# Performance work log

Measured on AMD Instinct MI355X. Metric: run time of the kernel, lower is better.

Reference implementation:

```python
import jax, jax.numpy as jnp
import numpy as np

NUM_USER = 150000
NUM_ITEM = 75000
N = NUM_USER + NUM_ITEM
D = 64
NNZ = 2000000
GCN_LAYER = 3
SCALE = 0.01


def setup_inputs() -> dict:
    key = jax.random.key(0)
    ks = jax.random.split(key, 8)
    user_emb = jax.random.normal(ks[0], (NUM_USER, D), dtype=jnp.float32) * 0.01
    item_emb = jax.random.normal(ks[1], (NUM_ITEM, D), dtype=jnp.float32) * 0.01
    eps_weight = jax.random.normal(ks[2], (D, D), dtype=jnp.float32)
    eps_bias = jnp.zeros((D,), dtype=jnp.float32)
    adj_rows = jax.random.randint(ks[3], (NNZ,), 0, N, dtype=jnp.int32)
    adj_cols = jax.random.randint(ks[4], (NNZ,), 0, N, dtype=jnp.int32)
    # small positive values, mimicking symmetric-normalized adjacency entries
    adj_vals = jax.random.uniform(ks[5], (NNZ,), dtype=jnp.float32) * 0.1
    noise1 = jax.random.normal(ks[6], (N, D), dtype=jnp.float32)
    noise2 = jax.random.normal(ks[7], (N, D), dtype=jnp.float32)
    return {
        "user_emb": user_emb, "item_emb": item_emb,
        "eps_weight": eps_weight, "eps_bias": eps_bias,
        "adj_rows": adj_rows, "adj_cols": adj_cols, "adj_vals": adj_vals,
        "noise1": noise1, "noise2": noise2, "gcn_layer": GCN_LAYER,
    }


def _spmm(rows, cols, vals, x):
    # y[r] = sum_{e: rows[e]==r} vals[e] * x[cols[e]]  -- sparse adj @ x
    msgs = vals[:, None] * x[cols]          # [nnz, D]
    return jax.ops.segment_sum(msgs, rows, num_segments=N)


def reference(user_emb, item_emb, eps_weight, eps_bias,
              adj_rows, adj_cols, adj_vals, noise1, noise2, gcn_layer):
    ego = jnp.concatenate([user_emb, item_emb], axis=0)  # [N, D]
    acc = jnp.zeros_like(ego)
    for _ in range(gcn_layer):
        ego = _spmm(adj_rows, adj_cols, adj_vals, ego)
        acc = acc + ego
    mean = acc / gcn_layer                               # mean over stacked layers
    logstd = mean @ eps_weight + eps_bias
    std = jnp.exp(logstd)
    view1 = mean + std * noise1 * SCALE
    view2 = mean + std * noise2 * SCALE
    return (mean, std, view1, view2)
```

## Files before the change

### kernel.cpp

```cpp
#include <hip/hip_runtime.h>
#include <math.h>

#define NUM_USER 150000
#define NUM_ITEM 75000
#define N_TOTAL  225000
#define D        64
#define LAYERS   3
#define SCALE    0.01f

#define BROWS    128
#define BSHIFT   7
#define NBUCK    1758
#define COLBITS  18
#define COLMASK  0x3FFFF
#define CHUNK    8192

__global__ void k_zero(int* __restrict__ p, int n) {
    for (int i = blockIdx.x * blockDim.x + threadIdx.x; i < n;
         i += gridDim.x * blockDim.x)
        p[i] = 0;
}

__global__ __launch_bounds__(256) void k_binhist(const int* __restrict__ rows,
                                                 int* __restrict__ bcnt, int nnz) {
    __shared__ int h[NBUCK];
    const int tid = threadIdx.x;
    for (int i = tid; i < NBUCK; i += 256) h[i] = 0;
    __syncthreads();
    for (int e = blockIdx.x * blockDim.x + tid; e < nnz;
         e += gridDim.x * blockDim.x)
        atomicAdd(&h[rows[e] >> BSHIFT], 1);
    __syncthreads();
    for (int i = tid; i < NBUCK; i += 256)
        if (h[i]) atomicAdd(&bcnt[i], h[i]);
}

__global__ __launch_bounds__(256) void k_bscan(const int* __restrict__ bcnt,
                                               int* __restrict__ boff,
                                               int* __restrict__ bcur,
                                               int n, int nnz) {
    __shared__ int sd[256];
    const int t = threadIdx.x;
    const int base = t * 8;
    int v[8], s = 0;
#pragma unroll
    for (int i = 0; i < 8; ++i) {
        int idx = base + i;
        v[i] = (idx < n) ? bcnt[idx] : 0;
        s += v[i];
    }
    sd[t] = s;
    __syncthreads();
#pragma unroll
    for (int o = 1; o < 256; o <<= 1) {
        int x = (t >= o) ? sd[t - o] : 0;
        __syncthreads();
        if (t >= o) sd[t] += x;
        __syncthreads();
    }
    int run = (t == 0) ? 0 : sd[t - 1];
#pragma unroll
    for (int i = 0; i < 8; ++i) {
        int idx = base + i;
        if (idx < n) { boff[idx] = run; bcur[idx] = run; }
        run += v[i];
    }
    if (t == 255) boff[n] = nnz;
}

__global__ __launch_bounds__(256) void k_binscatter(
        const int* __restrict__ rows, const int* __restrict__ cols,
        const float* __restrict__ vals, int* __restrict__ bcur,
        uint2* __restrict__ rec, int nnz) {
    __shared__ int hist[NBUCK];
    __shared__ int runs[NBUCK];
    const int tid = threadIdx.x;
    const int e0 = blockIdx.x * CHUNK;
    const int e1 = min(nnz, e0 + CHUNK);

    for (int i = tid; i < NBUCK; i += 256) hist[i] = 0;
    __syncthreads();
    for (int e = e0 + tid; e < e1; e += 256)
        atomicAdd(&hist[rows[e] >> BSHIFT], 1);
    __syncthreads();
    for (int i = tid; i < NBUCK; i += 256)
        runs[i] = hist[i] ? atomicAdd(&bcur[i], hist[i]) : 0;
    __syncthreads();
    for (int i = tid; i < NBUCK; i += 256) hist[i] = 0;
    __syncthreads();
    for (int e = e0 + tid; e < e1; e += 256) {
        const int r = rows[e];
        const int b = r >> BSHIFT;
        const int pos = runs[b] + atomicAdd(&hist[b], 1);
        const unsigned key = ((unsigned)(r & (BROWS - 1)) << COLBITS) |
                             (unsigned)cols[e];
        rec[pos] = make_uint2(key, __float_as_uint(vals[e]));
    }
}

__global__ __launch_bounds__(256) void k_bsort(
        const int* __restrict__ boff, const uint2* __restrict__ rec,
        uint2* __restrict__ srec, int* __restrict__ off, int nnz) {
    __shared__ int h[BROWS];
    __shared__ int sc[BROWS];
    __shared__ int cur[BROWS];
    const int b = blockIdx.x;
    const int tid = threadIdx.x;
    const int s = boff[b];
    const int e = boff[b + 1];

    if (tid < BROWS) h[tid] = 0;
    __syncthreads();
    for (int i = s + tid; i < e; i += 256)
        atomicAdd(&h[rec[i].x >> COLBITS], 1);
    __syncthreads();
    if (tid < BROWS) sc[tid] = h[tid];
    __syncthreads();
#pragma unroll
    for (int o = 1; o < BROWS; o <<= 1) {
        int x = 0;
        if (tid < BROWS && tid >= o) x = sc[tid - o];
        __syncthreads();
        if (tid < BROWS && tid >= o) sc[tid] += x;
        __syncthreads();
    }
    const int r0 = b * BROWS;
    if (tid < BROWS) {
        const int excl = sc[tid] - h[tid];
        cur[tid] = excl;
        const int r = r0 + tid;
        if (r < N_TOTAL) off[r] = s + excl;
    }
    __syncthreads();
    for (int i = s + tid; i < e; i += 256) {
        const uint2 u = rec[i];
        const int rl = u.x >> COLBITS;
        const int p = s + atomicAdd(&cur[rl], 1);
        srec[p] = u;
    }
    if (b == 0 && tid == 0) off[N_TOTAL] = nnz;
}

template <int MODE>
__global__ __launch_bounds__(256) void k_spmm_csr(
        const int* __restrict__ off, const uint2* __restrict__ srec,
        const float* __restrict__ ue, const float* __restrict__ ie,
        const float* __restrict__ xbuf,
        float* __restrict__ ybuf, float* __restrict__ accbuf, int nrows) {
    const int lane = threadIdx.x & 63;
    const int w0   = (blockIdx.x * blockDim.x + threadIdx.x) >> 6;
    const int nw   = (gridDim.x * blockDim.x) >> 6;

    for (int r0 = w0; r0 < nrows; r0 += nw) {
        const int r = __builtin_amdgcn_readfirstlane(r0);
        const int s = off[r];
        const int e = off[r + 1];
        float accv = 0.f;
        for (int base = s; base < e; base += 64) {
            const int nv = min(64, e - base);
            uint2 rv = make_uint2(0u, 0u);
            if (lane < nv) rv = srec[base + lane];
            int j = 0;
            for (; j + 4 <= nv; j += 4) {
                unsigned k0 = __shfl(rv.x, j),     k1 = __shfl(rv.x, j + 1);
                unsigned k2 = __shfl(rv.x, j + 2), k3 = __shfl(rv.x, j + 3);
                unsigned w0_ = __shfl(rv.y, j),     w1_ = __shfl(rv.y, j + 1);
                unsigned w2_ = __shfl(rv.y, j + 2), w3_ = __shfl(rv.y, j + 3);
                const int c0 = k0 & COLMASK, c1 = k1 & COLMASK;
                const int c2 = k2 & COLMASK, c3 = k3 & COLMASK;
                const float v0 = __uint_as_float(w0_), v1 = __uint_as_float(w1_);
                const float v2 = __uint_as_float(w2_), v3 = __uint_as_float(w3_);
                float x0, x1, x2, x3;
                if (MODE == 0) {
                    x0 = (c0 < NUM_USER) ? ue[c0 * D + lane] : ie[(c0 - NUM_USER) * D + lane];
                    x1 = (c1 < NUM_USER) ? ue[c1 * D + lane] : ie[(c1 - NUM_USER) * D + lane];
                    x2 = (c2 < NUM_USER) ? ue[c2 * D + lane] : ie[(c2 - NUM_USER) * D + lane];
                    x3 = (c3 < NUM_USER) ? ue[c3 * D + lane] : ie[(c3 - NUM_USER) * D + lane];
                } else {
                    x0 = xbuf[c0 * D + lane]; x1 = xbuf[c1 * D + lane];
                    x2 = xbuf[c2 * D + lane]; x3 = xbuf[c3 * D + lane];
                }
                accv = fmaf(v0, x0, accv);
                accv = fmaf(v1, x1, accv);
                accv = fmaf(v2, x2, accv);
                accv = fmaf(v3, x3, accv);
            }
            for (; j < nv; ++j) {
                const unsigned k = __shfl(rv.x, j);
                const unsigned w = __shfl(rv.y, j);
                const int c = k & COLMASK;
                const float v = __uint_as_float(w);
                float x;
                if (MODE == 0)
                    x = (c < NUM_USER) ? ue[c * D + lane] : ie[(c - NUM_USER) * D + lane];
                else
                    x = xbuf[c * D + lane];
                accv = fmaf(v, x, accv);
            }
        }
        const int o = r * D + lane;
        if (MODE == 0) accbuf[o] = accv;
        else           accbuf[o] += accv;
        if (MODE != 2) ybuf[o] = accv;
    }
}

__global__ __launch_bounds__(256) void k_final(
        float* __restrict__ mean_io,
        const float* __restrict__ W, const float* __restrict__ bias,
        const float* __restrict__ n1, const float* __restrict__ n2,
        float* __restrict__ std_out, float* __restrict__ v1,
        float* __restrict__ v2, int nrows) {
    const int   lane = threadIdx.x & 63;
    const float bj   = bias[lane];
    const int   w0   = (blockIdx.x * blockDim.x + threadIdx.x) >> 6;
    const int   nw   = (gridDim.x * blockDim.x) >> 6;

    float wreg[64];
#pragma unroll
    for (int k = 0; k < 64; ++k) wreg[k] = W[k * 64 + lane];

    for (int r = w0; r < nrows; r += nw) {
        const size_t base = (size_t)r * D;
        const float m = mean_io[base + lane] * (1.f / 3.f);
        float s = bj;
#pragma unroll
        for (int k = 0; k < 64; ++k) {
            const float mk = __uint_as_float(
                __builtin_amdgcn_readlane(__float_as_uint(m), k));
            s = fmaf(mk, wreg[k], s);
        }
        const float sd = __expf(s);
        mean_io[base + lane] = m;
        std_out[base + lane] = sd;
        v1[base + lane] = fmaf(sd * SCALE, n1[base + lane], m);
        v2[base + lane] = fmaf(sd * SCALE, n2[base + lane], m);
    }
}

extern "C" void kernel_launch(void* const* d_in, const int* in_sizes, int n_in,
                              void* d_out, int out_size, void* d_ws, size_t ws_size,
                              hipStream_t stream) {
    const float* ue   = (const float*)d_in[0];
    const float* ie   = (const float*)d_in[1];
    const float* W    = (const float*)d_in[2];
    const float* bias = (const float*)d_in[3];
    const int*   rows = (const int*)d_in[4];
    const int*   cols = (const int*)d_in[5];
    const float* vals = (const float*)d_in[6];
    const float* n1   = (const float*)d_in[7];
    const float* n2   = (const float*)d_in[8];
    const int    nnz  = in_sizes[4];

    float* out = (float*)d_out;
    const size_t ND = (size_t)N_TOTAL * D;

    float* acc  = out;
    float* stdo = out + ND;
    float* y1   = out + 2 * ND;
    float* y2   = out + 3 * ND;

    int*   ws   = (int*)stdo;
    int*   bcnt = ws;
    int*   boff = ws + 2048;
    int*   bcur = ws + 4096;
    int*   off  = ws + 6144;
    uint2* srec = (uint2*)(ws + 231424);
    uint2* rec  = (uint2*)(ws + 4231424);

    const int nb2 = (nnz + CHUNK - 1) / CHUNK;

    k_zero<<<7, 256, 0, stream>>>(bcnt, NBUCK);
    k_binhist<<<256, 256, 0, stream>>>(rows, bcnt, nnz);
    k_bscan<<<1, 256, 0, stream>>>(bcnt, boff, bcur, NBUCK, nnz);
    k_binscatter<<<nb2, 256, 0, stream>>>(rows, cols, vals, bcur, rec, nnz);
    k_bsort<<<NBUCK, 256, 0, stream>>>(boff, rec, srec, off, nnz);

    k_spmm_csr<0><<<2048, 256, 0, stream>>>(off, srec, ue, ie, nullptr,
                                            y1, acc, N_TOTAL);
    k_spmm_csr<1><<<2048, 256, 0, stream>>>(off, srec, nullptr, nullptr, y1,
                                            y2, acc, N_TOTAL);
    k_spmm_csr<2><<<2048, 256, 0, stream>>>(off, srec, nullptr, nullptr, y2,
                                            nullptr, acc, N_TOTAL);

    k_final<<<2048, 256, 0, stream>>>(acc, W, bias, n1, n2,
                                      stdo, y1, y2, N_TOTAL);
}
```

Measured before the change: 749.7 us.

## Vectorize SpMM gathers with float4 lanes and fuse layer accumulation into last layer

Each wavefront now splits into four 16-lane groups. Each group handles a different nonzero and loads a full 64-float row as float4, and a cross-group shuffle reduction combines the partial sums at the end. The separate accumulator read-modify-write in each layer is removed. The final layer instead adds the stored y1 and y2 outputs to its own result. This is meant to cut load instruction count, raise memory-level parallelism, and drop redundant global traffic, at the cost of extra shuffles and padded work on tail edges.

```diff
diff --git a/kernel.cpp b/kernel.cpp
--- a/kernel.cpp
+++ b/kernel.cpp
@@ -142,12 +142,15 @@
 }
 
 template <int MODE>
-__global__ __launch_bounds__(256) void k_spmm_csr(
+__global__ __launch_bounds__(256) void k_spmm(
         const int* __restrict__ off, const uint2* __restrict__ srec,
         const float* __restrict__ ue, const float* __restrict__ ie,
         const float* __restrict__ xbuf,
-        float* __restrict__ ybuf, float* __restrict__ accbuf, int nrows) {
+        const float* __restrict__ z1, const float* __restrict__ z2,
+        float* __restrict__ ybuf, int nrows) {
     const int lane = threadIdx.x & 63;
+    const int g    = lane >> 4;
+    const int q    = lane & 15;
     const int w0   = (blockIdx.x * blockDim.x + threadIdx.x) >> 6;
     const int nw   = (gridDim.x * blockDim.x) >> 6;
 
@@ -155,53 +158,70 @@
         const int r = __builtin_amdgcn_readfirstlane(r0);
         const int s = off[r];
         const int e = off[r + 1];
-        float accv = 0.f;
+        float ax = 0.f, ay = 0.f, az = 0.f, aw = 0.f;
         for (int base = s; base < e; base += 64) {
             const int nv = min(64, e - base);
             uint2 rv = make_uint2(0u, 0u);
             if (lane < nv) rv = srec[base + lane];
             int j = 0;
-            for (; j + 4 <= nv; j += 4) {
-                unsigned k0 = __shfl(rv.x, j),     k1 = __shfl(rv.x, j + 1);
-                unsigned k2 = __shfl(rv.x, j + 2), k3 = __shfl(rv.x, j + 3);
-                unsigned w0_ = __shfl(rv.y, j),     w1_ = __shfl(rv.y, j + 1);
-                unsigned w2_ = __shfl(rv.y, j + 2), w3_ = __shfl(rv.y, j + 3);
-                const int c0 = k0 & COLMASK, c1 = k1 & COLMASK;
-                const int c2 = k2 & COLMASK, c3 = k3 & COLMASK;
-                const float v0 = __uint_as_float(w0_), v1 = __uint_as_float(w1_);
-                const float v2 = __uint_as_float(w2_), v3 = __uint_as_float(w3_);
-                float x0, x1, x2, x3;
+            for (; j + 8 <= nv; j += 8) {
+                const unsigned k0 = __shfl(rv.x, j + g);
+                const unsigned m0 = __shfl(rv.y, j + g);
+                const unsigned k1 = __shfl(rv.x, j + 4 + g);
+                const unsigned m1 = __shfl(rv.y, j + 4 + g);
+                const int c0 = (int)(k0 & COLMASK);
+                const int c1 = (int)(k1 & COLMASK);
+                const float4 *p0, *p1;
                 if (MODE == 0) {
-                    x0 = (c0 < NUM_USER) ? ue[c0 * D + lane] : ie[(c0 - NUM_USER) * D + lane];
-                    x1 = (c1 < NUM_USER) ? ue[c1 * D + lane] : ie[(c1 - NUM_USER) * D + lane];
-                    x2 = (c2 < NUM_USER) ? ue[c2 * D + lane] : ie[(c2 - NUM_USER) * D + lane];
-                    x3 = (c3 < NUM_USER) ? ue[c3 * D + lane] : ie[(c3 - NUM_USER) * D + lane];
+                    p0 = (c0 < NUM_USER) ? (const float4*)ue + (size_t)c0 * 16
+                                         : (const float4*)ie + (size_t)(c0 - NUM_USER) * 16;
+                    p1 = (c1 < NUM_USER) ? (const float4*)ue + (size_t)c1 * 16
+                                         : (const float4*)ie + (size_t)(c1 - NUM_USER) * 16;
                 } else {
-                    x0 = xbuf[c0 * D + lane]; x1 = xbuf[c1 * D + lane];
-                    x2 = xbuf[c2 * D + lane]; x3 = xbuf[c3 * D + lane];
+                    p0 = (const float4*)xbuf + (size_t)c0 * 16;
+                    p1 = (const float4*)xbuf + (size_t)c1 * 16;
                 }
-                accv = fmaf(v0, x0, accv);
-                accv = fmaf(v1, x1, accv);
-                accv = fmaf(v2, x2, accv);
-                accv = fmaf(v3, x3, accv);
+                const float4 x0 = p0[q];
+                const float4 x1 = p1[q];
+                const float v0 = __uint_as_float(m0);
+                const float v1 = __uint_as_float(m1);
+                ax = fmaf(v0, x0.x, ax); ay = fmaf(v0, x0.y, ay);
+                az = fmaf(v0, x0.z, az); aw = fmaf(v0, x0.w, aw);
+                ax = fmaf(v1, x1.x, ax); ay = fmaf(v1, x1.y, ay);
+                az = fmaf(v1, x1.z, az); aw = fmaf(v1, x1.w, aw);
             }
-            for (; j < nv; ++j) {
-                const unsigned k = __shfl(rv.x, j);
-                const unsigned w = __shfl(rv.y, j);
-                const int c = k & COLMASK;
-                const float v = __uint_as_float(w);
-                float x;
-                if (MODE == 0)
-                    x = (c < NUM_USER) ? ue[c * D + lane] : ie[(c - NUM_USER) * D + lane];
-                else
-                    x = xbuf[c * D + lane];
-                accv = fmaf(v, x, accv);
+            for (; j < nv; j += 4) {
+                const unsigned k0 = __shfl(rv.x, j + g);
+                const unsigned m0 = __shfl(rv.y, j + g);
+                const int c0 = (int)(k0 & COLMASK);
+                const float4* p0;
+                if (MODE == 0) {
+                    p0 = (c0 < NUM_USER) ? (const float4*)ue + (size_t)c0 * 16
+                                         : (const float4*)ie + (size_t)(c0 - NUM_USER) * 16;
+                } else {
+                    p0 = (const float4*)xbuf + (size_t)c0 * 16;
+                }
+                const float4 x0 = p0[q];
+                const float v0 = __uint_as_float(m0);
+                ax = fmaf(v0, x0.x, ax); ay = fmaf(v0, x0.y, ay);
+                az = fmaf(v0, x0.z, az); aw = fmaf(v0, x0.w, aw);
             }
         }
-        const int o = r * D + lane;
-        if (MODE == 0) accbuf[o] = accv;
-        else           accbuf[o] += accv;
-        if (MODE != 2) ybuf[o] = accv;
+        ax += __shfl_xor(ax, 16); ay += __shfl_xor(ay, 16);
+        az += __shfl_xor(az, 16); aw += __shfl_xor(aw, 16);
+        ax += __shfl_xor(ax, 32); ay += __shfl_xor(ay, 32);
+        az += __shfl_xor(az, 32); aw += __shfl_xor(aw, 32);
+        if (lane < 16) {
+            float4 o4 = make_float4(ax, ay, az, aw);
+            const size_t o = (size_t)r * 16 + q;
+            if (MODE == 2) {
+                const float4 a1 = ((const float4*)z1)[o];
+                const float4 a2 = ((const float4*)z2)[o];
+                o4.x += a1.x + a2.x; o4.y += a1.y + a2.y;
+                o4.z += a1.z + a2.z; o4.w += a1.w + a2.w;
+            }
+            ((float4*)ybuf)[o] = o4;
+        }
     }
 }
 
@@ -276,12 +296,12 @@
     k_binscatter<<<nb2, 256, 0, stream>>>(rows, cols, vals, bcur, rec, nnz);
     k_bsort<<<NBUCK, 256, 0, stream>>>(boff, rec, srec, off, nnz);
 
-    k_spmm_csr<0><<<2048, 256, 0, stream>>>(off, srec, ue, ie, nullptr,
-                                            y1, acc, N_TOTAL);
-    k_spmm_csr<1><<<2048, 256, 0, stream>>>(off, srec, nullptr, nullptr, y1,
-                                            y2, acc, N_TOTAL);
-    k_spmm_csr<2><<<2048, 256, 0, stream>>>(off, srec, nullptr, nullptr, y2,
-                                            nullptr, acc, N_TOTAL);
+    k_spmm<0><<<2048, 256, 0, stream>>>(off, srec, ue, ie, nullptr,
+                                        nullptr, nullptr, y1, N_TOTAL);
+    k_spmm<1><<<2048, 256, 0, stream>>>(off, srec, nullptr, nullptr, y1,
+                                        nullptr, nullptr, y2, N_TOTAL);
+    k_spmm<2><<<2048, 256, 0, stream>>>(off, srec, nullptr, nullptr, y2,
+                                        y1, y2, acc, N_TOTAL);
 
     k_final<<<2048, 256, 0, stream>>>(acc, W, bias, n1, n2,
                                       stdo, y1, y2, N_TOTAL);
```

After: 717.4 us. -4.3%, faster.
